# Optimization experiments

Measured on AMD Instinct MI355X. Metric: run time of the kernel, lower is better.

The kernel has to match this reference:

```python
import jax, jax.numpy as jnp
import numpy as np

B, T, OMNI_D, STATIC_D = 128, 1024, 32, 16
H = 64            # hidden // 2 (per-direction GRU size)
HID = 128         # hidden
PHYS_LEN, N_PHYS = 432, 5


def _gelu(x):
    return jax.nn.gelu(x, approximate=False)  # torch GELU default = exact erf


def _ln(x, g, b, eps=1e-5):
    m = jnp.mean(x, -1, keepdims=True)
    v = jnp.var(x, -1, keepdims=True)
    return (x - m) / jnp.sqrt(v + eps) * g + b


def _gru_layer(x, Wih, Whh, bih, bhh, reverse):
    # PyTorch GRU cell math; x: [B,T,D] -> (outputs [B,T,H], h_final [B,H])
    Hh = Whh.shape[1]
    gi = jnp.einsum('btd,gd->btg', x, Wih) + bih  # precompute input projections
    if reverse:
        gi = gi[:, ::-1]
    gi = jnp.swapaxes(gi, 0, 1)  # [T,B,3H]
    h0 = jnp.zeros((x.shape[0], Hh), x.dtype)

    def step(h, g):
        gh = h @ Whh.T + bhh
        r = jax.nn.sigmoid(g[:, :Hh] + gh[:, :Hh])
        z = jax.nn.sigmoid(g[:, Hh:2 * Hh] + gh[:, Hh:2 * Hh])
        n = jnp.tanh(g[:, 2 * Hh:] + r * gh[:, 2 * Hh:])
        hn = (1 - z) * n + z * h
        return hn, hn

    hT, ys = jax.lax.scan(step, h0, gi)
    ys = jnp.swapaxes(ys, 0, 1)
    if reverse:
        ys = ys[:, ::-1]
    return ys, hT


def _conv1d(x, W, b, pad, dil):
    y = jax.lax.conv_general_dilated(x, W, (1,), [(pad, pad)], rhs_dilation=(dil,),
                                     dimension_numbers=('NCH', 'OIH', 'NCH'))
    return y + b[None, :, None]


def setup_inputs():
    key = jax.random.key(0)
    ks = iter(jax.random.split(key, 64))

    def rn(shape, s=0.05):
        return jax.random.normal(next(ks), shape, jnp.float32) * s

    inp = {
        'omni_seq': rn((B, T, OMNI_D), 1.0),
        'static_x': rn((B, STATIC_D), 1.0),
        'phys': rn((B, N_PHYS, PHYS_LEN), 1.0),
    }
    for l, d_in in (('l0', OMNI_D), ('l1', 2 * H)):
        for dr in ('f', 'b'):
            inp[f'gru_Wih_{l}{dr}'] = rn((3 * H, d_in))
            inp[f'gru_Whh_{l}{dr}'] = rn((3 * H, H))
            inp[f'gru_bih_{l}{dr}'] = rn((3 * H,))
            inp[f'gru_bhh_{l}{dr}'] = rn((3 * H,))
    inp['sm_W'] = rn((H, STATIC_D)); inp['sm_b'] = rn((H,))
    inp['sm_ln_g'] = jnp.ones((H,), jnp.float32); inp['sm_ln_b'] = jnp.zeros((H,), jnp.float32)
    inp['gate_W'] = rn((N_PHYS, H)); inp['gate_b'] = rn((N_PHYS,))
    inp['attn_in_W'] = rn((3 * N_PHYS, N_PHYS)); inp['attn_in_b'] = rn((3 * N_PHYS,))
    inp['attn_out_W'] = rn((N_PHYS, N_PHYS)); inp['attn_out_b'] = rn((N_PHYS,))
    for i, ksz in ((1, 3), (2, 5), (3, 9)):
        inp[f'conv{i}_W'] = rn((HID // 4, N_PHYS, ksz)); inp[f'conv{i}_b'] = rn((HID // 4,))
    FUSED = HID + H + 3 * (HID // 4)  # 288
    inp['head_ln_g'] = jnp.ones((FUSED,), jnp.float32); inp['head_ln_b'] = jnp.zeros((FUSED,), jnp.float32)
    inp['head_W1'] = rn((HID, FUSED)); inp['head_b1'] = rn((HID,))
    inp['head_W2'] = rn((PHYS_LEN, HID)); inp['head_b2'] = rn((PHYS_LEN,))
    return inp


def reference(omni_seq, static_x, phys,
              gru_Wih_l0f, gru_Whh_l0f, gru_bih_l0f, gru_bhh_l0f,
              gru_Wih_l0b, gru_Whh_l0b, gru_bih_l0b, gru_bhh_l0b,
              gru_Wih_l1f, gru_Whh_l1f, gru_bih_l1f, gru_bhh_l1f,
              gru_Wih_l1b, gru_Whh_l1b, gru_bih_l1b, gru_bhh_l1b,
              sm_W, sm_b, sm_ln_g, sm_ln_b, gate_W, gate_b,
              attn_in_W, attn_in_b, attn_out_W, attn_out_b,
              conv1_W, conv1_b, conv2_W, conv2_b, conv3_W, conv3_b,
              head_ln_g, head_ln_b, head_W1, head_b1, head_W2, head_b2):
    # --- bidirectional 2-layer GRU (eval mode: dropout off) ---
    y0f, _ = _gru_layer(omni_seq, gru_Wih_l0f, gru_Whh_l0f, gru_bih_l0f, gru_bhh_l0f, False)
    y0b, _ = _gru_layer(omni_seq, gru_Wih_l0b, gru_Whh_l0b, gru_bih_l0b, gru_bhh_l0b, True)
    x1 = jnp.concatenate([y0f, y0b], -1)
    _, hf = _gru_layer(x1, gru_Wih_l1f, gru_Whh_l1f, gru_bih_l1f, gru_bhh_l1f, False)
    _, hb = _gru_layer(x1, gru_Wih_l1b, gru_Whh_l1b, gru_bih_l1b, gru_bhh_l1b, True)
    omni_embed = jnp.concatenate([hf, hb], -1)  # h_omni[-2] ++ h_omni[-1], [B,128]
    # --- static MLP ---
    static_embed = _ln(_gelu(static_x @ sm_W.T + sm_b), sm_ln_g, sm_ln_b)  # [B,64]
    # --- gating on phys channels ---
    gates = jax.nn.sigmoid(static_embed @ gate_W.T + gate_b)[..., None]  # [B,5,1]
    p = phys * gates  # [B,5,432]
    # --- tiny MHA: embed_dim=5, 5 heads, head_dim=1 -> scale = 1/sqrt(1) = 1 ---
    pt = jnp.swapaxes(p, 1, 2)  # [B,432,5]
    qkv = pt @ attn_in_W.T + attn_in_b
    E = N_PHYS
    q, k, v = qkv[..., :E], qkv[..., E:2 * E], qkv[..., 2 * E:]
    scores = jnp.einsum('bih,bjh->bhij', q, k)  # [B,5,432,432]
    attn = jax.nn.softmax(scores, -1)
    ao = jnp.einsum('bhij,bjh->bih', attn, v)
    ao = ao @ attn_out_W.T + attn_out_b  # out_proj
    p = jnp.swapaxes(ao, 1, 2)  # [B,5,432]
    # --- dilated conv branches + GELU + adaptive avg pool (= mean over length) ---
    c1 = _gelu(_conv1d(p, conv1_W, conv1_b, 1, 1)).mean(-1)
    c2 = _gelu(_conv1d(p, conv2_W, conv2_b, 2, 2)).mean(-1)
    c3 = _gelu(_conv1d(p, conv3_W, conv3_b, 4, 4)).mean(-1)
    fused = jnp.concatenate([omni_embed, static_embed, c1, c2, c3], 1)  # [B,288]
    h = _ln(fused, head_ln_g, head_ln_b)
    h = _gelu(h @ head_W1.T + head_b1)  # dropout off in eval
    return h @ head_W2.T + head_b2  # [B,432]
```

## Files before the change

kernel.cpp:

```cpp
#include <hip/hip_runtime.h>
#include <stdint.h>

#define B_ 128
#define T_ 1024
#define BT_ (B_*T_)
#define H_ 64
#define G_ 192
#define PL_ 432
#define NP_ 5
#define FUSED_ 288
#define N_IN 41

typedef unsigned short u16;
typedef __attribute__((ext_vector_type(8))) short bf16x8;
typedef __attribute__((ext_vector_type(4))) float f32x4;
typedef _Float16 h2 __attribute__((ext_vector_type(2)));
typedef _Float16 h8 __attribute__((ext_vector_type(8)));

__device__ inline float bf2f(u16 u){ union{float f; unsigned int i;} c; c.i = ((unsigned int)u)<<16; return c.f; }
__device__ inline u16 f2bf(float f){ unsigned int u = __float_as_uint(f); unsigned int r = (u + 0x7fffu + ((u>>16)&1u))>>16; return (u16)r; }
__device__ inline _Float16 bf2h(u16 u){ return (_Float16)bf2f(u); }
__device__ inline float sigm(float x){ return 1.f/(1.f+__expf(-x)); }
__device__ inline float tanh_(float x){ float t = __expf(fminf(fmaxf(2.f*x,-30.f),30.f)); return (t-1.f)/(t+1.f); }
__device__ inline float gelu_(float x){ return 0.5f*x*(1.f + erff(x*0.70710678118654752f)); }
__device__ inline float wredsum(float v){
  #pragma unroll
  for(int o=32;o>0;o>>=1) v += __shfl_xor(v,o);
  return v;
}

#if __has_builtin(__builtin_amdgcn_fdot2)
__device__ inline float dot2(h2 a, h2 b, float c){ return __builtin_amdgcn_fdot2(a, b, c, false); }
#else
__device__ inline float dot2(h2 a, h2 b, float c){ return c + (float)a.x*(float)b.x + (float)a.y*(float)b.y; }
#endif

struct CvtArgs {
  const void* src[N_IN];
  unsigned dstOff[N_IN];
  unsigned cnt[N_IN];
  unsigned blkStart[N_IN+1];
};

__global__ __launch_bounds__(256) void convert_k(CvtArgs a, u16* __restrict__ dst){
  const bool isbf = (((const u16*)a.src[21])[0] == 0x3F80u);
  int b = blockIdx.x;
  int lo = 0, hi = N_IN;
  while (hi - lo > 1){ int mid = (lo+hi)>>1; if (a.blkStart[mid] <= (unsigned)b) lo = mid; else hi = mid; }
  const int i = lo;
  const unsigned lb = (unsigned)b - a.blkStart[i];
  const unsigned n = a.cnt[i];
  u16* d = dst + a.dstOff[i];
  if (isbf){
    const u16* s = (const u16*)a.src[i];
    #pragma unroll
    for(int e=0;e<8;e++){ unsigned idx = lb*2048u + e*256u + threadIdx.x; if (idx < n) d[idx] = s[idx]; }
  } else {
    const float* s = (const float*)a.src[i];
    #pragma unroll
    for(int e=0;e<8;e++){ unsigned idx = lb*2048u + e*256u + threadIdx.x; if (idx < n) d[idx] = f2bf(s[idx]); }
  }
}

template<int K>
__global__ __launch_bounds__(256) void gi_gemm(const u16* __restrict__ A,
    const u16* __restrict__ Wf, const u16* __restrict__ Wb,
    const u16* __restrict__ biasF, const u16* __restrict__ biasB,
    u16* __restrict__ out)
{
  const int wv = threadIdx.x >> 6, lane = threadIdx.x & 63;
  const int l15 = lane & 15, quad = lane >> 4;
  const size_t mBase = (size_t)blockIdx.x*64 + wv*16;

  bf16x8 afr[K/32];
  #pragma unroll
  for(int kc=0;kc<K/32;kc++)
    afr[kc] = *(const bf16x8*)(A + (mBase + l15)*K + kc*32 + quad*8);

  #pragma unroll
  for(int half=0; half<2; ++half){
    const u16* W    = half ? Wb : Wf;
    const u16* bias = half ? biasB : biasF;
    u16* o = out + (size_t)half * BT_ * G_;
    for(int nt=0; nt<12; ++nt){
      int n = nt*16 + l15;
      f32x4 acc = {0.f,0.f,0.f,0.f};
      #pragma unroll
      for(int kc=0;kc<K/32;kc++){
        bf16x8 bfr = *(const bf16x8*)(W + n*K + kc*32 + quad*8);
        acc = __builtin_amdgcn_mfma_f32_16x16x32_bf16(bfr, afr[kc], acc, 0,0,0);
      }
      ushort4 bb = *(const ushort4*)(bias + nt*16 + quad*4);
      ushort4 pk;
      pk.x = f2bf(acc[0] + bf2f(bb.x));
      pk.y = f2bf(acc[1] + bf2f(bb.y));
      pk.z = f2bf(acc[2] + bf2f(bb.z));
      pk.w = f2bf(acc[3] + bf2f(bb.w));
      *(ushort4*)(o + (mBase + l15)*G_ + nt*16 + quad*4) = pk;
    }
  }
}

__global__ __launch_bounds__(64)
__attribute__((amdgpu_waves_per_eu(1,1)))
void recur(const u16* __restrict__ gi,
    const u16* __restrict__ WhF, const u16* __restrict__ WhB,
    const u16* __restrict__ bhF, const u16* __restrict__ bhB,
    u16* __restrict__ y_x1, float* __restrict__ hfin, int layer)
{
  const int chain = blockIdx.x;
  const int dir = chain >> 7;
  const int b = chain & 127;
  const int j = threadIdx.x;
  const u16* Wh = dir ? WhB : WhF;
  const u16* bh = dir ? bhB : bhF;

  h2 wr[32], wz[32], wn[32];
  #pragma unroll
  for(int k8=0;k8<8;k8++){
    uint4 q;
    q = *(const uint4*)(Wh + (size_t)j*64 + k8*8);
    wr[4*k8+0] = (h2){bf2h((u16)(q.x&0xffffu)), bf2h((u16)(q.x>>16))};
    wr[4*k8+1] = (h2){bf2h((u16)(q.y&0xffffu)), bf2h((u16)(q.y>>16))};
    wr[4*k8+2] = (h2){bf2h((u16)(q.z&0xffffu)), bf2h((u16)(q.z>>16))};
    wr[4*k8+3] = (h2){bf2h((u16)(q.w&0xffffu)), bf2h((u16)(q.w>>16))};
    q = *(const uint4*)(Wh + (size_t)(64+j)*64 + k8*8);
    wz[4*k8+0] = (h2){bf2h((u16)(q.x&0xffffu)), bf2h((u16)(q.x>>16))};
    wz[4*k8+1] = (h2){bf2h((u16)(q.y&0xffffu)), bf2h((u16)(q.y>>16))};
    wz[4*k8+2] = (h2){bf2h((u16)(q.z&0xffffu)), bf2h((u16)(q.z>>16))};
    wz[4*k8+3] = (h2){bf2h((u16)(q.w&0xffffu)), bf2h((u16)(q.w>>16))};
    q = *(const uint4*)(Wh + (size_t)(128+j)*64 + k8*8);
    wn[4*k8+0] = (h2){bf2h((u16)(q.x&0xffffu)), bf2h((u16)(q.x>>16))};
    wn[4*k8+1] = (h2){bf2h((u16)(q.y&0xffffu)), bf2h((u16)(q.y>>16))};
    wn[4*k8+2] = (h2){bf2h((u16)(q.z&0xffffu)), bf2h((u16)(q.z>>16))};
    wn[4*k8+3] = (h2){bf2h((u16)(q.w&0xffffu)), bf2h((u16)(q.w>>16))};
  }
  const float bhr = bf2f(bh[j]), bhz = bf2f(bh[64+j]), bhn = bf2f(bh[128+j]);

  __shared__ __align__(16) u16 giLds[2][3072];
  __shared__ _Float16 hSf[64];
  h8* hS8 = (h8*)hSf;
  hSf[j] = (_Float16)0.f;

  const u16* giC = gi + (size_t)chain * T_ * G_;

  auto issue_chunk = [&](int c, int buf){
    int tbase = dir ? (1008 - c*16) : (c*16);
    const u16* src = giC + (size_t)tbase*G_ + j*8;
    u16* dst = &giLds[buf][0];
    #pragma unroll
    for(int i=0;i<6;i++){
      __builtin_amdgcn_global_load_lds(
        (const __attribute__((address_space(1))) void*)(src + i*512),
        (__attribute__((address_space(3))) void*)(dst + i*512), 16, 0, 0);
    }
  };

  issue_chunk(0, 0);

  float h = 0.f;
  for(int c=0; c<64; ++c){
    asm volatile("s_waitcnt vmcnt(0)" ::: "memory");
    if (c < 63) issue_chunk(c+1, (c+1)&1);
    const u16* gbuf = &giLds[c&1][0];
    #pragma unroll 2
    for(int ls=0; ls<16; ++ls){
      int row = dir ? (15-ls) : ls;
      const u16* rowp = gbuf + row*G_;
      float r0=bhr, r1=0.f, z0=bhz, z1=0.f, n0=bhn, n1=0.f;
      #pragma unroll
      for(int k=0;k<8;k++){
        h8 hv = hS8[k];
        h2 p0 = __builtin_shufflevector(hv, hv, 0, 1);
        h2 p1 = __builtin_shufflevector(hv, hv, 2, 3);
        h2 p2 = __builtin_shufflevector(hv, hv, 4, 5);
        h2 p3 = __builtin_shufflevector(hv, hv, 6, 7);
        r0 = dot2(wr[4*k+0], p0, r0); r1 = dot2(wr[4*k+1], p1, r1);
        r0 = dot2(wr[4*k+2], p2, r0); r1 = dot2(wr[4*k+3], p3, r1);
        z0 = dot2(wz[4*k+0], p0, z0); z1 = dot2(wz[4*k+1], p1, z1);
        z0 = dot2(wz[4*k+2], p2, z0); z1 = dot2(wz[4*k+3], p3, z1);
        n0 = dot2(wn[4*k+0], p0, n0); n1 = dot2(wn[4*k+1], p1, n1);
        n0 = dot2(wn[4*k+2], p2, n0); n1 = dot2(wn[4*k+3], p3, n1);
      }
      float gr = bf2f(rowp[j]), gz = bf2f(rowp[64+j]), gn = bf2f(rowp[128+j]);

      float r  = sigm(gr + (r0+r1));
      float z  = sigm(gz + (z0+z1));
      float nn = tanh_(gn + r*(n0+n1));
      h = (1.f - z)*nn + z*h;

      hSf[j] = (_Float16)h;

      if (layer == 0){
        int s = c*16 + ls;
        int t = dir ? (T_-1-s) : s;
        y_x1[((size_t)b*T_ + t)*128 + dir*64 + j] = f2bf(h);
      }
    }
  }
  if (layer == 1) hfin[b*FUSED_ + dir*64 + j] = h;
}

__global__ __launch_bounds__(448) void staticqkv_k(const u16* __restrict__ sx,
   const u16* __restrict__ smW, const u16* __restrict__ smb,
   const u16* __restrict__ lng, const u16* __restrict__ lnb,
   const u16* __restrict__ gW, const u16* __restrict__ gb,
   const u16* __restrict__ phys, const u16* __restrict__ aW,
   const u16* __restrict__ ab,
   float* __restrict__ fused, float* __restrict__ qkv)
{
  int b = blockIdx.x, tid = threadIdx.x;
  __shared__ float gS[5];
  if (tid < 64){
    int j = tid;
    float xr[16];
    #pragma unroll
    for(int k=0;k<16;k++) xr[k] = bf2f(sx[b*16+k]);
    float acc = bf2f(smb[j]);
    #pragma unroll
    for(int k=0;k<16;k++) acc += xr[k]*bf2f(smW[j*16+k]);
    float xg = gelu_(acc);
    float m = wredsum(xg)*(1.f/64.f);
    float d = xg - m;
    float v = wredsum(d*d)*(1.f/64.f);
    float se = d*rsqrtf(v+1e-5f)*bf2f(lng[j]) + bf2f(lnb[j]);
    fused[b*FUSED_ + 128 + j] = se;
    #pragma unroll
    for(int i=0;i<5;i++){
      float p = se*bf2f(gW[i*64+j]);
      float s = wredsum(p);
      if (j == 0) gS[i] = sigm(s + bf2f(gb[i]));
    }
  }
  __syncthreads();
  int l = tid;
  if (l < PL_){
    float pv[5];
    #pragma unroll
    for(int i=0;i<5;i++) pv[i] = bf2f(phys[((size_t)b*5+i)*PL_ + l]) * gS[i];
    #pragma unroll
    for(int c=0;c<15;c++){
      float a = bf2f(ab[c]);
      #pragma unroll
      for(int i=0;i<5;i++) a += pv[i]*bf2f(aW[c*5+i]);
      qkv[((size_t)b*15+c)*PL_ + l] = a;
    }
  }
}

__global__ __launch_bounds__(256) void attn_k(const float* __restrict__ qkv,
                                              float* __restrict__ ao)
{
  int h = blockIdx.x, b = blockIdx.y;
  int tid = threadIdx.x;
  __shared__ float kS[PL_], vS[PL_];
  __shared__ float red[32];
  const float* qb = qkv + ((size_t)b*15 + h)*PL_;
  const float* kb = qkv + ((size_t)b*15 + 5 + h)*PL_;
  const float* vb = qkv + ((size_t)b*15 + 10 + h)*PL_;
  for(int j=tid;j<PL_;j+=256){ kS[j]=kb[j]; vS[j]=vb[j]; }
  __syncthreads();
  float lmax=-1e30f, lmin=1e30f;
  for(int j=tid;j<PL_;j+=256){ float kv=kS[j]; lmax=fmaxf(lmax,kv); lmin=fminf(lmin,kv); }
  #pragma unroll
  for(int o=32;o>0;o>>=1){ lmax=fmaxf(lmax,__shfl_xor(lmax,o)); lmin=fminf(lmin,__shfl_xor(lmin,o)); }
  int wv = tid>>6;
  if ((tid&63)==0){ red[wv]=lmax; red[8+wv]=lmin; }
  __syncthreads();
  if (tid==0){
    float mx=red[0], mn=red[8];
    for(int i=1;i<4;i++){ mx=fmaxf(mx,red[i]); mn=fminf(mn,red[8+i]); }
    red[16]=mx; red[17]=mn;
  }
  __syncthreads();
  float kmx=red[16], kmn=red[17];
  for(int i=tid;i<PL_;i+=256){
    float s = qb[i];
    float m = fmaxf(s*kmx, s*kmn);
    float den=0.f, num=0.f;
    #pragma unroll 4
    for(int j=0;j<PL_;j++){
      float e = __expf(s*kS[j]-m);
      den += e; num += e*vS[j];
    }
    ao[((size_t)b*PL_+i)*5 + h] = num/den;
  }
}

template<int KS, int DIL, int PAD>
__device__ inline void do_conv(const float* pS, const u16* Wc, const u16* bc,
                               float* fused, int b, int o, int p, int cslot)
{
  const int Lout = PL_ + 2*PAD - DIL*(KS-1);
  float w[5][KS];
  #pragma unroll
  for(int i=0;i<5;i++)
    #pragma unroll
    for(int t=0;t<KS;t++) w[i][t] = bf2f(Wc[(o*5+i)*KS + t]);
  float bias = bf2f(bc[o]);
  float acc = 0.f;
  for(int l=p; l<Lout; l+=8){
    float s = bias;
    #pragma unroll
    for(int t=0;t<KS;t++){
      int idx = l - PAD + t*DIL;
      if (idx >= 0 && idx < PL_){
        #pragma unroll
        for(int i=0;i<5;i++) s += w[i][t]*pS[i*PL_ + idx];
      }
    }
    acc += gelu_(s);
  }
  #pragma unroll
  for(int off=1;off<8;off<<=1) acc += __shfl_xor(acc,off);
  if (p == 0) fused[b*FUSED_ + 192 + cslot*32 + o] = acc/(float)Lout;
}

__global__ __launch_bounds__(256) void projconv_k(const float* __restrict__ ao,
  const u16* __restrict__ oW, const u16* __restrict__ ob,
  const u16* __restrict__ W1c, const u16* __restrict__ b1c,
  const u16* __restrict__ W2c, const u16* __restrict__ b2c,
  const u16* __restrict__ W3c, const u16* __restrict__ b3c,
  float* __restrict__ fused)
{
  int b = blockIdx.x, tid = threadIdx.x;
  __shared__ float pS[5*PL_];
  for(int l=tid; l<PL_; l+=256){
    float a[5];
    #pragma unroll
    for(int hh=0;hh<5;hh++) a[hh] = ao[((size_t)b*PL_+l)*5 + hh];
    #pragma unroll
    for(int c=0;c<5;c++){
      float s = bf2f(ob[c]);
      #pragma unroll
      for(int hh=0;hh<5;hh++) s += a[hh]*bf2f(oW[c*5+hh]);
      pS[c*PL_ + l] = s;
    }
  }
  __syncthreads();
  int o = tid >> 3, p = tid & 7;
  do_conv<3,1,1>(pS, W1c, b1c, fused, b, o, p, 0);
  do_conv<5,2,2>(pS, W2c, b2c, fused, b, o, p, 1);
  do_conv<9,4,4>(pS, W3c, b3c, fused, b, o, p, 2);
}

__global__ __launch_bounds__(448) void head_k(const float* __restrict__ fused,
   const u16* __restrict__ lng, const u16* __restrict__ lnb,
   const u16* __restrict__ W1, const u16* __restrict__ b1,
   const u16* __restrict__ W2, const u16* __restrict__ b2,
   void* __restrict__ out, const u16* __restrict__ detect)
{
  const bool isbf = (detect[0] == 0x3F80u);
  int b = blockIdx.x, tid = threadIdx.x;
  __shared__ float fS[FUSED_];
  __shared__ float hS[128];
  __shared__ float red[32];
  float v = (tid < FUSED_) ? fused[b*FUSED_ + tid] : 0.f;
  float s1 = wredsum(v);
  float s2 = wredsum(v*v);
  int wv = tid>>6;
  if ((tid&63)==0){ red[wv]=s1; red[8+wv]=s2; }
  __syncthreads();
  if (tid==0){
    float S=0.f, SS=0.f;
    for(int i=0;i<7;i++){ S+=red[i]; SS+=red[8+i]; }
    float m = S/288.f;
    red[16]=m; red[17]=SS/288.f - m*m;
  }
  __syncthreads();
  float m = red[16], var = red[17];
  if (tid < FUSED_) fS[tid] = (v-m)*rsqrtf(var+1e-5f)*bf2f(lng[tid]) + bf2f(lnb[tid]);
  __syncthreads();
  if (tid < 128){
    float a = bf2f(b1[tid]);
    const u16* wr = W1 + (size_t)tid*FUSED_;
    #pragma unroll
    for(int k8=0;k8<36;k8++){
      uint4 q = *(const uint4*)(wr + k8*8);
      a += fS[8*k8+0]*bf2f((u16)(q.x&0xffffu)) + fS[8*k8+1]*bf2f((u16)(q.x>>16))
         + fS[8*k8+2]*bf2f((u16)(q.y&0xffffu)) + fS[8*k8+3]*bf2f((u16)(q.y>>16))
         + fS[8*k8+4]*bf2f((u16)(q.z&0xffffu)) + fS[8*k8+5]*bf2f((u16)(q.z>>16))
         + fS[8*k8+6]*bf2f((u16)(q.w&0xffffu)) + fS[8*k8+7]*bf2f((u16)(q.w>>16));
    }
    hS[tid] = gelu_(a);
  }
  __syncthreads();
  if (tid < PL_){
    float a = bf2f(b2[tid]);
    const u16* wr = W2 + (size_t)tid*128;
    #pragma unroll
    for(int k8=0;k8<16;k8++){
      uint4 q = *(const uint4*)(wr + k8*8);
      a += hS[8*k8+0]*bf2f((u16)(q.x&0xffffu)) + hS[8*k8+1]*bf2f((u16)(q.x>>16))
         + hS[8*k8+2]*bf2f((u16)(q.y&0xffffu)) + hS[8*k8+3]*bf2f((u16)(q.y>>16))
         + hS[8*k8+4]*bf2f((u16)(q.z&0xffffu)) + hS[8*k8+5]*bf2f((u16)(q.z>>16))
         + hS[8*k8+6]*bf2f((u16)(q.w&0xffffu)) + hS[8*k8+7]*bf2f((u16)(q.w>>16));
    }
    size_t oi = (size_t)b*PL_ + tid;
    if (isbf) ((u16*)out)[oi] = f2bf(a);
    else      ((float*)out)[oi] = a;
  }
}

extern "C" void kernel_launch(void* const* d_in, const int* in_sizes, int n_in,
                              void* d_out, int out_size, void* d_ws, size_t ws_size,
                              hipStream_t stream)
{
  static const unsigned cnts[N_IN] = {
    4194304, 2048, 276480,
    6144, 12288, 192, 192,
    6144, 12288, 192, 192,
    24576, 12288, 192, 192,
    24576, 12288, 192, 192,
    1024, 64, 64, 64,
    320, 5,
    75, 15,
    25, 5,
    480, 32, 800, 32, 1440, 32,
    288, 288,
    36864, 128, 55296, 432
  };

  char* ws = (char*)d_ws;
  size_t off = 0;
  auto alloc = [&](size_t bytes){ size_t o = off; off = (off + bytes + 255) & ~(size_t)255; return o; };

  CvtArgs ca;
  const u16* cin[N_IN];
  unsigned totalBlocks = 0;
  for (int i=0;i<N_IN;i++){
    ca.src[i] = d_in[i];
    ca.cnt[i] = cnts[i];
    size_t o = alloc((size_t)cnts[i]*2);
    ca.dstOff[i] = (unsigned)(o/2);
    cin[i] = (const u16*)(ws + o);
    ca.blkStart[i] = totalBlocks;
    totalBlocks += (cnts[i] + 2047u)/2048u;
  }
  ca.blkStart[N_IN] = totalBlocks;
  u16* canon = (u16*)ws;

  u16*   gi    = (u16*)  (ws + alloc((size_t)2*BT_*G_*2));
  u16*   x1    = (u16*)  (ws + alloc((size_t)BT_*128*2));
  float* fused = (float*)(ws + alloc((size_t)B_*FUSED_*4));
  float* qkv   = (float*)(ws + alloc((size_t)B_*15*PL_*4));
  float* ao    = (float*)(ws + alloc((size_t)B_*PL_*5*4));
  (void)ws_size; (void)in_sizes; (void)n_in; (void)out_size;

  convert_k<<<totalBlocks, 256, 0, stream>>>(ca, canon);

  gi_gemm<32><<<BT_/64, 256, 0, stream>>>(cin[0], cin[3], cin[7], cin[5], cin[9], gi);
  recur<<<256, 64, 0, stream>>>(gi, cin[4], cin[8], cin[6], cin[10], x1, nullptr, 0);
  gi_gemm<128><<<BT_/64, 256, 0, stream>>>(x1, cin[11], cin[15], cin[13], cin[17], gi);
  recur<<<256, 64, 0, stream>>>(gi, cin[12], cin[16], cin[14], cin[18], nullptr, fused, 1);
  staticqkv_k<<<128, 448, 0, stream>>>(cin[1], cin[19], cin[20], cin[21], cin[22],
                                       cin[23], cin[24], cin[2], cin[25], cin[26],
                                       fused, qkv);
  attn_k<<<dim3(5,128), 256, 0, stream>>>(qkv, ao);
  projconv_k<<<128, 256, 0, stream>>>(ao, cin[27], cin[28], cin[29], cin[30],
                                      cin[31], cin[32], cin[33], cin[34], fused);
  head_k<<<128, 448, 0, stream>>>(fused, cin[35], cin[36], cin[37], cin[38], cin[39], cin[40],
                                  d_out, (const u16*)d_in[21]);
}
```

Before: 1.273 ms.

## Fuse static/attention/conv branch into layer-1 GEMM launch and skip input conversions

Merges the static-embedding, gated QKV, attention, out-projection and conv branch into one per-batch block body that keeps intermediates in shared memory. Those 128 blocks run in the same launch as the layer-1 input-projection GEMM, so they overlap with it and three launches plus the qkv/ao global round trips disappear. The large omni_seq and phys inputs are no longer converted by convert_k; they are read raw and converted inline. As a trade-off, attention now runs one block per batch looping over 5 heads, which is less parallel than the previous 5x128 grid and could lengthen the critical path if those blocks finish after the GEMM blocks.

Result: faster. 1.233 ms (-3.2%).

```diff
diff --git a/kernel.cpp b/kernel.cpp
--- a/kernel.cpp
+++ b/kernel.cpp
@@ -10,6 +10,7 @@
 #define NP_ 5
 #define FUSED_ 288
 #define N_IN 41
+#define NSTATIC 128
 
 typedef unsigned short u16;
 typedef __attribute__((ext_vector_type(8))) short bf16x8;
@@ -62,20 +63,28 @@
   }
 }
 
-template<int K>
-__global__ __launch_bounds__(256) void gi_gemm(const u16* __restrict__ A,
+__global__ __launch_bounds__(256) void gi_gemm0(const void* __restrict__ Araw,
     const u16* __restrict__ Wf, const u16* __restrict__ Wb,
     const u16* __restrict__ biasF, const u16* __restrict__ biasB,
-    u16* __restrict__ out)
-{
+    u16* __restrict__ out, const u16* __restrict__ detect)
+{
+  const bool isbf = (detect[0] == 0x3F80u);
   const int wv = threadIdx.x >> 6, lane = threadIdx.x & 63;
   const int l15 = lane & 15, quad = lane >> 4;
   const size_t mBase = (size_t)blockIdx.x*64 + wv*16;
 
-  bf16x8 afr[K/32];
-  #pragma unroll
-  for(int kc=0;kc<K/32;kc++)
-    afr[kc] = *(const bf16x8*)(A + (mBase + l15)*K + kc*32 + quad*8);
+  bf16x8 afr;
+  if (isbf){
+    afr = *(const bf16x8*)((const u16*)Araw + (mBase + l15)*32 + quad*8);
+  } else {
+    const float* af = (const float*)Araw + (mBase + l15)*32 + quad*8;
+    float4 f0 = *(const float4*)af;
+    float4 f1 = *(const float4*)(af+4);
+    union { bf16x8 v; u16 e[8]; } u_;
+    u_.e[0]=f2bf(f0.x); u_.e[1]=f2bf(f0.y); u_.e[2]=f2bf(f0.z); u_.e[3]=f2bf(f0.w);
+    u_.e[4]=f2bf(f1.x); u_.e[5]=f2bf(f1.y); u_.e[6]=f2bf(f1.z); u_.e[7]=f2bf(f1.w);
+    afr = u_.v;
+  }
 
   #pragma unroll
   for(int half=0; half<2; ++half){
@@ -85,11 +94,8 @@
     for(int nt=0; nt<12; ++nt){
       int n = nt*16 + l15;
       f32x4 acc = {0.f,0.f,0.f,0.f};
-      #pragma unroll
-      for(int kc=0;kc<K/32;kc++){
-        bf16x8 bfr = *(const bf16x8*)(W + n*K + kc*32 + quad*8);
-        acc = __builtin_amdgcn_mfma_f32_16x16x32_bf16(bfr, afr[kc], acc, 0,0,0);
-      }
+      bf16x8 bfr = *(const bf16x8*)(W + n*32 + quad*8);
+      acc = __builtin_amdgcn_mfma_f32_16x16x32_bf16(bfr, afr, acc, 0,0,0);
       ushort4 bb = *(const ushort4*)(bias + nt*16 + quad*4);
       ushort4 pk;
       pk.x = f2bf(acc[0] + bf2f(bb.x));
@@ -201,24 +207,55 @@
   if (layer == 1) hfin[b*FUSED_ + dir*64 + j] = h;
 }
 
-__global__ __launch_bounds__(448) void staticqkv_k(const u16* __restrict__ sx,
-   const u16* __restrict__ smW, const u16* __restrict__ smb,
-   const u16* __restrict__ lng, const u16* __restrict__ lnb,
-   const u16* __restrict__ gW, const u16* __restrict__ gb,
-   const u16* __restrict__ phys, const u16* __restrict__ aW,
-   const u16* __restrict__ ab,
-   float* __restrict__ fused, float* __restrict__ qkv)
-{
-  int b = blockIdx.x, tid = threadIdx.x;
+template<int KS, int DIL, int PAD>
+__device__ inline void do_conv(const float* pS, const u16* Wc, const u16* bc,
+                               float* fused, int b, int o, int p, int cslot)
+{
+  const int Lout = PL_ + 2*PAD - DIL*(KS-1);
+  float w[5][KS];
+  #pragma unroll
+  for(int i=0;i<5;i++)
+    #pragma unroll
+    for(int t=0;t<KS;t++) w[i][t] = bf2f(Wc[(o*5+i)*KS + t]);
+  float bias = bf2f(bc[o]);
+  float acc = 0.f;
+  for(int l=p; l<Lout; l+=8){
+    float s = bias;
+    #pragma unroll
+    for(int t=0;t<KS;t++){
+      int idx = l - PAD + t*DIL;
+      if (idx >= 0 && idx < PL_){
+        #pragma unroll
+        for(int i=0;i<5;i++) s += w[i][t]*pS[i*PL_ + idx];
+      }
+    }
+    acc += gelu_(s);
+  }
+  #pragma unroll
+  for(int off=1;off<8;off<<=1) acc += __shfl_xor(acc,off);
+  if (p == 0) fused[b*FUSED_ + 192 + cslot*32 + o] = acc/(float)Lout;
+}
+
+__device__ void static_body(int b, int tid,
+   const u16* sx, const u16* smW, const u16* smb,
+   const u16* lng, const u16* lnb, const u16* gW, const u16* gb,
+   const void* physRaw, const u16* aW, const u16* ab,
+   const u16* oW, const u16* ob,
+   const u16* W1c, const u16* b1c, const u16* W2c, const u16* b2c,
+   const u16* W3c, const u16* b3c,
+   float* fused, bool isbf)
+{
+  __shared__ float qS[15*PL_];
+  __shared__ float aoS[PL_*5];
   __shared__ float gS[5];
+  __shared__ float redS[40];
+  __shared__ float kmS[5], knS[5];
+
   if (tid < 64){
     int j = tid;
-    float xr[16];
-    #pragma unroll
-    for(int k=0;k<16;k++) xr[k] = bf2f(sx[b*16+k]);
     float acc = bf2f(smb[j]);
     #pragma unroll
-    for(int k=0;k<16;k++) acc += xr[k]*bf2f(smW[j*16+k]);
+    for(int k=0;k<16;k++) acc += bf2f(sx[b*16+k])*bf2f(smW[j*16+k]);
     float xg = gelu_(acc);
     float m = wredsum(xg)*(1.f/64.f);
     float d = xg - m;
@@ -233,102 +270,73 @@
     }
   }
   __syncthreads();
-  int l = tid;
-  if (l < PL_){
+
+  for(int l=tid; l<PL_; l+=256){
     float pv[5];
     #pragma unroll
-    for(int i=0;i<5;i++) pv[i] = bf2f(phys[((size_t)b*5+i)*PL_ + l]) * gS[i];
+    for(int i=0;i<5;i++){
+      size_t idx = ((size_t)b*5+i)*PL_ + l;
+      float pr = isbf ? bf2f(((const u16*)physRaw)[idx]) : ((const float*)physRaw)[idx];
+      pv[i] = pr * gS[i];
+    }
     #pragma unroll
     for(int c=0;c<15;c++){
       float a = bf2f(ab[c]);
       #pragma unroll
       for(int i=0;i<5;i++) a += pv[i]*bf2f(aW[c*5+i]);
-      qkv[((size_t)b*15+c)*PL_ + l] = a;
-    }
-  }
-}
-
-__global__ __launch_bounds__(256) void attn_k(const float* __restrict__ qkv,
-                                              float* __restrict__ ao)
-{
-  int h = blockIdx.x, b = blockIdx.y;
-  int tid = threadIdx.x;
-  __shared__ float kS[PL_], vS[PL_];
-  __shared__ float red[32];
-  const float* qb = qkv + ((size_t)b*15 + h)*PL_;
-  const float* kb = qkv + ((size_t)b*15 + 5 + h)*PL_;
-  const float* vb = qkv + ((size_t)b*15 + 10 + h)*PL_;
-  for(int j=tid;j<PL_;j+=256){ kS[j]=kb[j]; vS[j]=vb[j]; }
-  __syncthreads();
-  float lmax=-1e30f, lmin=1e30f;
-  for(int j=tid;j<PL_;j+=256){ float kv=kS[j]; lmax=fmaxf(lmax,kv); lmin=fminf(lmin,kv); }
-  #pragma unroll
-  for(int o=32;o>0;o>>=1){ lmax=fmaxf(lmax,__shfl_xor(lmax,o)); lmin=fminf(lmin,__shfl_xor(lmin,o)); }
+      qS[c*PL_ + l] = a;
+    }
+  }
+  __syncthreads();
+
+  float mx[5], mn[5];
+  #pragma unroll
+  for(int h=0;h<5;h++){ mx[h]=-1e30f; mn[h]=1e30f; }
+  for(int jj=tid; jj<PL_; jj+=256){
+    #pragma unroll
+    for(int h=0;h<5;h++){ float kv=qS[(5+h)*PL_+jj]; mx[h]=fmaxf(mx[h],kv); mn[h]=fminf(mn[h],kv); }
+  }
+  #pragma unroll
+  for(int o=32;o>0;o>>=1){
+    #pragma unroll
+    for(int h=0;h<5;h++){ mx[h]=fmaxf(mx[h],__shfl_xor(mx[h],o)); mn[h]=fminf(mn[h],__shfl_xor(mn[h],o)); }
+  }
   int wv = tid>>6;
-  if ((tid&63)==0){ red[wv]=lmax; red[8+wv]=lmin; }
-  __syncthreads();
-  if (tid==0){
-    float mx=red[0], mn=red[8];
-    for(int i=1;i<4;i++){ mx=fmaxf(mx,red[i]); mn=fminf(mn,red[8+i]); }
-    red[16]=mx; red[17]=mn;
-  }
-  __syncthreads();
-  float kmx=red[16], kmn=red[17];
-  for(int i=tid;i<PL_;i+=256){
-    float s = qb[i];
-    float m = fmaxf(s*kmx, s*kmn);
-    float den=0.f, num=0.f;
-    #pragma unroll 4
-    for(int j=0;j<PL_;j++){
-      float e = __expf(s*kS[j]-m);
-      den += e; num += e*vS[j];
-    }
-    ao[((size_t)b*PL_+i)*5 + h] = num/den;
-  }
-}
-
-template<int KS, int DIL, int PAD>
-__device__ inline void do_conv(const float* pS, const u16* Wc, const u16* bc,
-                               float* fused, int b, int o, int p, int cslot)
-{
-  const int Lout = PL_ + 2*PAD - DIL*(KS-1);
-  float w[5][KS];
-  #pragma unroll
-  for(int i=0;i<5;i++)
-    #pragma unroll
-    for(int t=0;t<KS;t++) w[i][t] = bf2f(Wc[(o*5+i)*KS + t]);
-  float bias = bf2f(bc[o]);
-  float acc = 0.f;
-  for(int l=p; l<Lout; l+=8){
-    float s = bias;
-    #pragma unroll
-    for(int t=0;t<KS;t++){
-      int idx = l - PAD + t*DIL;
-      if (idx >= 0 && idx < PL_){
-        #pragma unroll
-        for(int i=0;i<5;i++) s += w[i][t]*pS[i*PL_ + idx];
+  if ((tid&63)==0){
+    #pragma unroll
+    for(int h=0;h<5;h++){ redS[wv*10+h]=mx[h]; redS[wv*10+5+h]=mn[h]; }
+  }
+  __syncthreads();
+  if (tid < 5){
+    float a=redS[tid], c=redS[5+tid];
+    for(int w2=1;w2<4;w2++){ a=fmaxf(a,redS[w2*10+tid]); c=fminf(c,redS[w2*10+5+tid]); }
+    kmS[tid]=a; knS[tid]=c;
+  }
+  __syncthreads();
+
+  for(int i=tid; i<PL_; i+=256){
+    #pragma unroll
+    for(int h=0;h<5;h++){
+      float s = qS[h*PL_+i];
+      float m = fmaxf(s*kmS[h], s*knS[h]);
+      const float* kR = &qS[(5+h)*PL_];
+      const float* vR = &qS[(10+h)*PL_];
+      float den=0.f, num=0.f;
+      #pragma unroll 4
+      for(int j2=0;j2<PL_;j2++){
+        float e = __expf(s*kR[j2]-m);
+        den += e; num += e*vR[j2];
       }
-    }
-    acc += gelu_(s);
-  }
-  #pragma unroll
-  for(int off=1;off<8;off<<=1) acc += __shfl_xor(acc,off);
-  if (p == 0) fused[b*FUSED_ + 192 + cslot*32 + o] = acc/(float)Lout;
-}
-
-__global__ __launch_bounds__(256) void projconv_k(const float* __restrict__ ao,
-  const u16* __restrict__ oW, const u16* __restrict__ ob,
-  const u16* __restrict__ W1c, const u16* __restrict__ b1c,
-  const u16* __restrict__ W2c, const u16* __restrict__ b2c,
-  const u16* __restrict__ W3c, const u16* __restrict__ b3c,
-  float* __restrict__ fused)
-{
-  int b = blockIdx.x, tid = threadIdx.x;
-  __shared__ float pS[5*PL_];
+      aoS[i*5+h] = num/den;
+    }
+  }
+  __syncthreads();
+
+  float* pS = qS;
   for(int l=tid; l<PL_; l+=256){
     float a[5];
     #pragma unroll
-    for(int hh=0;hh<5;hh++) a[hh] = ao[((size_t)b*PL_+l)*5 + hh];
+    for(int hh=0;hh<5;hh++) a[hh] = aoS[l*5+hh];
     #pragma unroll
     for(int c=0;c<5;c++){
       float s = bf2f(ob[c]);
@@ -338,10 +346,66 @@
     }
   }
   __syncthreads();
+
   int o = tid >> 3, p = tid & 7;
   do_conv<3,1,1>(pS, W1c, b1c, fused, b, o, p, 0);
   do_conv<5,2,2>(pS, W2c, b2c, fused, b, o, p, 1);
   do_conv<9,4,4>(pS, W3c, b3c, fused, b, o, p, 2);
+}
+
+__global__ __launch_bounds__(256) void gemm128_static_k(const u16* __restrict__ A,
+    const u16* __restrict__ Wf, const u16* __restrict__ Wb,
+    const u16* __restrict__ biasF, const u16* __restrict__ biasB,
+    u16* __restrict__ out,
+    const u16* __restrict__ sx, const u16* __restrict__ smW, const u16* __restrict__ smb,
+    const u16* __restrict__ lng, const u16* __restrict__ lnb,
+    const u16* __restrict__ gW, const u16* __restrict__ gb,
+    const void* __restrict__ physRaw, const u16* __restrict__ aW, const u16* __restrict__ ab,
+    const u16* __restrict__ oW, const u16* __restrict__ ob,
+    const u16* __restrict__ W1c, const u16* __restrict__ b1c,
+    const u16* __restrict__ W2c, const u16* __restrict__ b2c,
+    const u16* __restrict__ W3c, const u16* __restrict__ b3c,
+    float* __restrict__ fused, const u16* __restrict__ detect)
+{
+  const bool isbf = (detect[0] == 0x3F80u);
+  if (blockIdx.x < NSTATIC){
+    static_body(blockIdx.x, threadIdx.x, sx, smW, smb, lng, lnb, gW, gb,
+                physRaw, aW, ab, oW, ob, W1c, b1c, W2c, b2c, W3c, b3c,
+                fused, isbf);
+    return;
+  }
+  const int bid = blockIdx.x - NSTATIC;
+  const int wv = threadIdx.x >> 6, lane = threadIdx.x & 63;
+  const int l15 = lane & 15, quad = lane >> 4;
+  const size_t mBase = (size_t)bid*64 + wv*16;
+
+  bf16x8 afr[4];
+  #pragma unroll
+  for(int kc=0;kc<4;kc++)
+    afr[kc] = *(const bf16x8*)(A + (mBase + l15)*128 + kc*32 + quad*8);
+
+  #pragma unroll
+  for(int half=0; half<2; ++half){
+    const u16* W    = half ? Wb : Wf;
+    const u16* bias = half ? biasB : biasF;
+    u16* o = out + (size_t)half * BT_ * G_;
+    for(int nt=0; nt<12; ++nt){
+      int n = nt*16 + l15;
+      f32x4 acc = {0.f,0.f,0.f,0.f};
+      #pragma unroll
+      for(int kc=0;kc<4;kc++){
+        bf16x8 bfr = *(const bf16x8*)(W + n*128 + kc*32 + quad*8);
+        acc = __builtin_amdgcn_mfma_f32_16x16x32_bf16(bfr, afr[kc], acc, 0,0,0);
+      }
+      ushort4 bb = *(const ushort4*)(bias + nt*16 + quad*4);
+      ushort4 pk;
+      pk.x = f2bf(acc[0] + bf2f(bb.x));
+      pk.y = f2bf(acc[1] + bf2f(bb.y));
+      pk.z = f2bf(acc[2] + bf2f(bb.z));
+      pk.w = f2bf(acc[3] + bf2f(bb.w));
+      *(ushort4*)(o + (mBase + l15)*G_ + nt*16 + quad*4) = pk;
+    }
+  }
 }
 
 __global__ __launch_bounds__(448) void head_k(const float* __restrict__ fused,
@@ -435,7 +499,7 @@
     ca.dstOff[i] = (unsigned)(o/2);
     cin[i] = (const u16*)(ws + o);
     ca.blkStart[i] = totalBlocks;
-    totalBlocks += (cnts[i] + 2047u)/2048u;
+    if (i != 0 && i != 2) totalBlocks += (cnts[i] + 2047u)/2048u;
   }
   ca.blkStart[N_IN] = totalBlocks;
   u16* canon = (u16*)ws;
@@ -443,22 +507,20 @@
   u16*   gi    = (u16*)  (ws + alloc((size_t)2*BT_*G_*2));
   u16*   x1    = (u16*)  (ws + alloc((size_t)BT_*128*2));
   float* fused = (float*)(ws + alloc((size_t)B_*FUSED_*4));
-  float* qkv   = (float*)(ws + alloc((size_t)B_*15*PL_*4));
-  float* ao    = (float*)(ws + alloc((size_t)B_*PL_*5*4));
   (void)ws_size; (void)in_sizes; (void)n_in; (void)out_size;
 
   convert_k<<<totalBlocks, 256, 0, stream>>>(ca, canon);
 
-  gi_gemm<32><<<BT_/64, 256, 0, stream>>>(cin[0], cin[3], cin[7], cin[5], cin[9], gi);
+  gi_gemm0<<<BT_/64, 256, 0, stream>>>(d_in[0], cin[3], cin[7], cin[5], cin[9], gi,
+                                       (const u16*)d_in[21]);
   recur<<<256, 64, 0, stream>>>(gi, cin[4], cin[8], cin[6], cin[10], x1, nullptr, 0);
-  gi_gemm<128><<<BT_/64, 256, 0, stream>>>(x1, cin[11], cin[15], cin[13], cin[17], gi);
+  gemm128_static_k<<<BT_/64 + NSTATIC, 256, 0, stream>>>(x1,
+      cin[11], cin[15], cin[13], cin[17], gi,
+      cin[1], cin[19], cin[20], cin[21], cin[22], cin[23], cin[24],
+      d_in[2], cin[25], cin[26],
+      cin[27], cin[28], cin[29], cin[30], cin[31], cin[32], cin[33], cin[34],
+      fused, (const u16*)d_in[21]);
   recur<<<256, 64, 0, stream>>>(gi, cin[12], cin[16], cin[14], cin[18], nullptr, fused, 1);
-  staticqkv_k<<<128, 448, 0, stream>>>(cin[1], cin[19], cin[20], cin[21], cin[22],
-                                       cin[23], cin[24], cin[2], cin[25], cin[26],
-                                       fused, qkv);
-  attn_k<<<dim3(5,128), 256, 0, stream>>>(qkv, ao);
-  projconv_k<<<128, 256, 0, stream>>>(ao, cin[27], cin[28], cin[29], cin[30],
-                                      cin[31], cin[32], cin[33], cin[34], fused);
   head_k<<<128, 448, 0, stream>>>(fused, cin[35], cin[36], cin[37], cin[38], cin[39], cin[40],
                                   d_out, (const u16*)d_in[21]);
 }
```
